# Optimization experiments

Hardware: AMD Instinct MI355X
Metric: run time of the kernel (lower is better)

Reference implementation:

```python
import jax, jax.numpy as jnp
import numpy as np

N_NODES = 100000
N_EDGES = 1000000
IN_CH, HID_CH, N_CLS = 128, 64, 40


def setup_inputs() -> dict:
    key = jax.random.key(0)
    ks = jax.random.split(key, 8)
    x = jax.random.normal(ks[0], (N_NODES, IN_CH), dtype=jnp.float32)
    edge_index = jax.random.randint(ks[1], (2, N_EDGES), 0, N_NODES, dtype=jnp.int32)
    # Glorot-ish scaled weights (ARMAConv init_weight / root_weight, K=1 stack squeezed)
    w1_init = jax.random.normal(ks[2], (IN_CH, HID_CH), dtype=jnp.float32) / np.sqrt(IN_CH)
    w1_root = jax.random.normal(ks[3], (IN_CH, HID_CH), dtype=jnp.float32) / np.sqrt(IN_CH)
    b1 = jnp.zeros((HID_CH,), dtype=jnp.float32)
    w2_init = jax.random.normal(ks[4], (HID_CH, N_CLS), dtype=jnp.float32) / np.sqrt(HID_CH)
    w2_root = jax.random.normal(ks[5], (HID_CH, N_CLS), dtype=jnp.float32) / np.sqrt(HID_CH)
    b2 = jnp.zeros((N_CLS,), dtype=jnp.float32)
    return {"x": x, "edge_index": edge_index,
            "w1_init": w1_init, "w1_root": w1_root, "b1": b1,
            "w2_init": w2_init, "w2_root": w2_root, "b2": b2}


def _arma_layer(x, row, col, norm, w_init, w_root, bias):
    # ARMAConv, num_stacks=1, num_layers=1, shared_weights=True, eval mode (dropout=id):
    # out = relu( A_hat @ (x W_init) + x W_root + b ), mean over the single stack.
    h = x @ w_init                           # [N, F_out]
    msg = norm[:, None] * h[row]             # gather from source nodes, [E, F_out]
    agg = jax.ops.segment_sum(msg, col, num_segments=N_NODES)  # scatter-add at targets
    return jax.nn.relu(agg + x @ w_root + bias)


def reference(x, edge_index, w1_init, w1_root, b1, w2_init, w2_root, b2):
    row, col = edge_index[0], edge_index[1]
    # gcn_norm, add_self_loops=False: deg over targets, norm = d^-1/2[row] * d^-1/2[col]
    deg = jax.ops.segment_sum(jnp.ones((row.shape[0],), x.dtype), col, num_segments=N_NODES)
    dinv = jnp.where(deg > 0, jax.lax.rsqrt(jnp.maximum(deg, 1e-12)), jnp.zeros_like(deg))
    norm = dinv[row] * dinv[col]
    h = _arma_layer(x, row, col, norm, w1_init, w1_root, b1)
    h = jax.nn.relu(h)  # BiARMA relu; dropout identity in eval
    return _arma_layer(h, row, col, norm, w2_init, w2_root, b2)
```

## Files before the change

### kernel.cpp

```cpp
#include <hip/hip_runtime.h>

#define N_NODES 100000
#define N_EDGES 1000000
#define IN_CH 128
#define HID_CH 64
#define N_CLS 40

#define NBUCK 782

static inline int cdiv(int a, int b) { return (a + b - 1) / b; }

using bf16x8 = __attribute__((ext_vector_type(8))) short;
using f32x4  = __attribute__((ext_vector_type(4))) float;

__device__ __forceinline__ unsigned pack_bf2(float a, float b) {
    unsigned ua = __float_as_uint(a), ub = __float_as_uint(b);
    ua += 0x7fffu + ((ua >> 16) & 1u);
    ub += 0x7fffu + ((ub >> 16) & 1u);
    return (ua >> 16) | (ub & 0xffff0000u);
}
__device__ __forceinline__ unsigned short bf16_of(float a) {
    unsigned ua = __float_as_uint(a);
    ua += 0x7fffu + ((ua >> 16) & 1u);
    return (unsigned short)(ua >> 16);
}
__device__ __forceinline__ float bf_lo(unsigned u) { return __uint_as_float(u << 16); }
__device__ __forceinline__ float bf_hi(unsigned u) { return __uint_as_float(u & 0xffff0000u); }


__global__ __launch_bounds__(256)
void bucket_count_wconv_kernel(const int* __restrict__ cols, int* __restrict__ gcount, int E,
                               const float* __restrict__ w1i, const float* __restrict__ w1r,
                               const float* __restrict__ w2i, const float* __restrict__ w2r,
                               unsigned* __restrict__ wtgA, unsigned* __restrict__ wtgB) {
    if (blockIdx.x >= 128) {
        if (wtgA == nullptr) return;
        int id = (blockIdx.x - 128) * 256 + threadIdx.x;
        if (id < 128 * 64) {
            int c = id >> 6, kp = id & 63;
            int k = kp * 2;
            const float* W = (c < 64) ? w1i : w1r;
            int cc = (c < 64) ? c : c - 64;
            float a = W[(size_t)k * 64 + cc];
            float b = W[(size_t)(k + 1) * 64 + cc];
            wtgA[c * 64 + kp] = pack_bf2(a, b);
        } else if (id < 128 * 64 + 80 * 32) {
            int j = id - 128 * 64;
            int c = j >> 5, kp = j & 31;
            int k = kp * 2;
            const float* W = (c < 40) ? w2i : w2r;
            int cc = (c < 40) ? c : c - 40;
            float a = W[(size_t)k * 40 + cc];
            float b = W[(size_t)(k + 1) * 40 + cc];
            wtgB[c * 32 + kp] = pack_bf2(a, b);
        }
        return;
    }
    __shared__ int hist[NBUCK];
    for (int i = threadIdx.x; i < NBUCK; i += 256) hist[i] = 0;
    __syncthreads();
    int per = (E + 127) / 128;
    int s = blockIdx.x * per;
    int e = min(E, s + per);
    for (int j = s + threadIdx.x; j < e; j += 256)
        atomicAdd(&hist[cols[j] >> 7], 1);
    __syncthreads();
    for (int i = threadIdx.x; i < NBUCK; i += 256)
        if (hist[i]) atomicAdd(&gcount[i], hist[i]);
}


__global__ __launch_bounds__(1024)
void scan_bucket_kernel(const int* __restrict__ gcount, int* __restrict__ boff,
                        int* __restrict__ gcursor, int* __restrict__ offsets) {
    __shared__ int part[1024];
    int t = threadIdx.x;
    part[t] = (t < NBUCK) ? gcount[t] : 0;
    __syncthreads();
    for (int off = 1; off < 1024; off <<= 1) {
        int v = (t >= off) ? part[t - off] : 0;
        __syncthreads();
        part[t] += v;
        __syncthreads();
    }
    int excl = (t > 0) ? part[t - 1] : 0;
    if (t < NBUCK) { boff[t] = excl; gcursor[t] = excl; }
    if (t == NBUCK) { boff[NBUCK] = excl; offsets[N_NODES] = excl; }
}


__global__ __launch_bounds__(256)
void bucket_scatter_kernel(const int* __restrict__ rows, const int* __restrict__ cols,
                           int* __restrict__ gcursor, int* __restrict__ pedge, int E) {
    __shared__ int cur[NBUCK];
    for (int i = threadIdx.x; i < NBUCK; i += 256) cur[i] = 0;
    __syncthreads();
    int per = (E + gridDim.x - 1) / gridDim.x;
    int s = blockIdx.x * per;
    int e = min(E, s + per);
    for (int j = s + threadIdx.x; j < e; j += 256)
        atomicAdd(&cur[cols[j] >> 7], 1);
    __syncthreads();
    for (int i = threadIdx.x; i < NBUCK; i += 256) {
        int h = cur[i];
        cur[i] = h ? atomicAdd(&gcursor[i], h) : 0;
    }
    __syncthreads();
    for (int j = s + threadIdx.x; j < e; j += 256) {
        int c = cols[j];
        int pos = atomicAdd(&cur[c >> 7], 1);
        pedge[pos] = (rows[j] << 7) | (c & 127);
    }
}


__global__ __launch_bounds__(256)
void bucket_sort_kernel(const int* __restrict__ boff, const int* __restrict__ pedge,
                        int* __restrict__ srow, int* __restrict__ offsets,
                        float* __restrict__ dinv) {
    __shared__ int cnt[128];
    __shared__ int scn[128];
    __shared__ int cur[128];
    int b = blockIdx.x, t = threadIdx.x;
    if (t < 128) cnt[t] = 0;
    __syncthreads();
    int e0 = boff[b], e1 = boff[b + 1];
    for (int j = e0 + t; j < e1; j += 256)
        atomicAdd(&cnt[pedge[j] & 127], 1);
    __syncthreads();
    if (t < 128) scn[t] = cnt[t];
    __syncthreads();
    for (int off = 1; off < 128; off <<= 1) {
        int v = 0;
        if (t < 128 && t >= off) v = scn[t - off];
        __syncthreads();
        if (t < 128) scn[t] += v;
        __syncthreads();
    }
    if (t < 128) {
        int excl = (t > 0) ? scn[t - 1] : 0;
        cur[t] = excl;
        int node = b * 128 + t;
        if (node < N_NODES) {
            offsets[node] = e0 + excl;
            dinv[node] = cnt[t] ? rsqrtf((float)cnt[t]) : 0.f;
        }
    }
    __syncthreads();
    for (int j = e0 + t; j < e1; j += 256) {
        int p = pedge[j];
        int pos = atomicAdd(&cur[p & 127], 1);
        srow[e0 + pos] = p >> 7;
    }
}


template<int K, int C1, int C2>
__launch_bounds__(256, 6)
__global__ void gemm_fat_kernel(const float* __restrict__ X,
                                const unsigned short* __restrict__ WT,
                                const float* __restrict__ Bias,
                                const float* __restrict__ dinv,
                                unsigned short* __restrict__ Y1b,
                                float* __restrict__ Y2, int N) {
    constexpr int CT = C1 + C2;
    constexpr int NT = CT / 16;
    constexpr int KS = K / 32;
    constexpr int S16 = 72;
    constexpr int SF  = 68;
    static_assert(CT % 16 == 0 && K % 32 == 0 && C1 % 8 == 0 && C2 % 4 == 0, "shape");

    __shared__ unsigned short eb16[4 * 16 * S16];
    __shared__ float          ebf [4 * 16 * SF];

    const int tid = threadIdx.x;
    const int wave = tid >> 6;
    const int lane = tid & 63;
    const int m = lane & 15;
    const int quad = lane >> 4;
    const int r0 = blockIdx.x * 64;

    const int rowA = r0 + wave * 16 + m;
    const bool va = (rowA < N);
    const float* xr = X + (size_t)rowA * K + quad * 8;

    union AFrag { uint4 u; bf16x8 v; } af[KS];
#pragma unroll
    for (int ks = 0; ks < KS; ++ks) {
        float4 v0 = make_float4(0.f, 0.f, 0.f, 0.f);
        float4 v1 = make_float4(0.f, 0.f, 0.f, 0.f);
        if (va) {
            v0 = *reinterpret_cast<const float4*>(xr + ks * 32);
            v1 = *reinterpret_cast<const float4*>(xr + ks * 32 + 4);
        }
        af[ks].u.x = pack_bf2(v0.x, v0.y);
        af[ks].u.y = pack_bf2(v0.z, v0.w);
        af[ks].u.z = pack_bf2(v1.x, v1.y);
        af[ks].u.w = pack_bf2(v1.z, v1.w);
    }

    f32x4 acc[NT];
#pragma unroll
    for (int t = 0; t < NT; ++t) acc[t] = (f32x4){0.f, 0.f, 0.f, 0.f};
#pragma unroll
    for (int ks = 0; ks < KS; ++ks) {
#pragma unroll
        for (int t = 0; t < NT; ++t) {
            bf16x8 b = *reinterpret_cast<const bf16x8*>(&WT[(size_t)(t * 16 + m) * K + ks * 32 + quad * 8]);
            acc[t] = __builtin_amdgcn_mfma_f32_16x16x32_bf16(af[ks].v, b, acc[t], 0, 0, 0);
        }
    }

    const int rbase0 = r0 + wave * 16;
    const int rbase = rbase0 + quad * 4;
    float dv[4];
#pragma unroll
    for (int reg = 0; reg < 4; ++reg)
        dv[reg] = (rbase + reg < N) ? dinv[rbase + reg] : 0.f;

    unsigned short* e16 = &eb16[wave * 16 * S16];
    float* ef = &ebf[wave * 16 * SF];
#pragma unroll
    for (int t = 0; t < NT; ++t) {
        int c = t * 16 + m;
        if (c < C1) {
#pragma unroll
            for (int reg = 0; reg < 4; ++reg)
                e16[(quad * 4 + reg) * S16 + c] = bf16_of(acc[t][reg] * dv[reg]);
        } else {
            float b = Bias[c - C1];
#pragma unroll
            for (int reg = 0; reg < 4; ++reg)
                ef[(quad * 4 + reg) * SF + (c - C1)] = acc[t][reg] + b;
        }
    }
    __syncthreads();

    constexpr int SEG1 = C1 / 8;
    for (int it = 0; it < (16 * SEG1 + 63) / 64; ++it) {
        int task = lane + it * 64;
        if (task < 16 * SEG1) {
            int row = task / SEG1, seg = task - row * SEG1;
            int gr = rbase0 + row;
            if (gr < N) {
                uint4 v = *reinterpret_cast<const uint4*>(&eb16[(wave * 16 + row) * S16 + seg * 8]);
                *reinterpret_cast<uint4*>(&Y1b[(size_t)gr * C1 + seg * 8]) = v;
            }
        }
    }
    constexpr int SEG2 = C2 / 4;
    for (int it = 0; it < (16 * SEG2 + 63) / 64; ++it) {
        int task = lane + it * 64;
        if (task < 16 * SEG2) {
            int row = task / SEG2, seg = task - row * SEG2;
            int gr = rbase0 + row;
            if (gr < N) {
                float4 v = *reinterpret_cast<const float4*>(&ebf[(wave * 16 + row) * SF + seg * 4]);
                *reinterpret_cast<float4*>(&Y2[(size_t)gr * C2 + seg * 4]) = v;
            }
        }
    }
}


__global__ __launch_bounds__(256)
void pull_gemm_fused_kernel(const int* __restrict__ offsets,
                            const int* __restrict__ srow,
                            const float* __restrict__ dinv,
                            const unsigned* __restrict__ H,
                            const float* __restrict__ Yp,
                            const unsigned short* __restrict__ WT2,
                            const float* __restrict__ Bias2,
                            unsigned short* __restrict__ H2,
                            float* __restrict__ Outp,
                            int N) {
    constexpr int KP = 36;
    __shared__ unsigned xb[16 * KP];
    __shared__ unsigned short e16[16 * 48];
    __shared__ float epif[16 * 44];

    const int tid = threadIdx.x;
    const int node16 = tid >> 4;
    const int lane16 = tid & 15;
    const int gnode = blockIdx.x * 16 + node16;

    float4 h1 = make_float4(0.f, 0.f, 0.f, 0.f);
    if (gnode < N) {
        int e0 = offsets[gnode];
        int e1 = offsets[gnode + 1];
        float dc = dinv[gnode];
        float4 acc = make_float4(0.f, 0.f, 0.f, 0.f);
        int j = e0;
        for (; j + 4 <= e1; j += 4) {
            int r0 = srow[j + 0];
            int r1 = srow[j + 1];
            int r2 = srow[j + 2];
            int r3 = srow[j + 3];
            uint2 u0 = *reinterpret_cast<const uint2*>(&H[(size_t)r0 * 32 + lane16 * 2]);
            uint2 u1 = *reinterpret_cast<const uint2*>(&H[(size_t)r1 * 32 + lane16 * 2]);
            uint2 u2 = *reinterpret_cast<const uint2*>(&H[(size_t)r2 * 32 + lane16 * 2]);
            uint2 u3 = *reinterpret_cast<const uint2*>(&H[(size_t)r3 * 32 + lane16 * 2]);
            acc.x += (bf_lo(u0.x) + bf_lo(u1.x)) + (bf_lo(u2.x) + bf_lo(u3.x));
            acc.y += (bf_hi(u0.x) + bf_hi(u1.x)) + (bf_hi(u2.x) + bf_hi(u3.x));
            acc.z += (bf_lo(u0.y) + bf_lo(u1.y)) + (bf_lo(u2.y) + bf_lo(u3.y));
            acc.w += (bf_hi(u0.y) + bf_hi(u1.y)) + (bf_hi(u2.y) + bf_hi(u3.y));
        }
        for (; j < e1; ++j) {
            int r = srow[j];
            uint2 u = *reinterpret_cast<const uint2*>(&H[(size_t)r * 32 + lane16 * 2]);
            acc.x += bf_lo(u.x);
            acc.y += bf_hi(u.x);
            acc.z += bf_lo(u.y);
            acc.w += bf_hi(u.y);
        }
        float4 y = *reinterpret_cast<const float4*>(&Yp[(size_t)gnode * 64 + lane16 * 4]);
        h1.x = fmaxf(fmaf(dc, acc.x, y.x), 0.f);
        h1.y = fmaxf(fmaf(dc, acc.y, y.y), 0.f);
        h1.z = fmaxf(fmaf(dc, acc.z, y.z), 0.f);
        h1.w = fmaxf(fmaf(dc, acc.w, y.w), 0.f);
    }
    xb[node16 * KP + lane16 * 2]     = pack_bf2(h1.x, h1.y);
    xb[node16 * KP + lane16 * 2 + 1] = pack_bf2(h1.z, h1.w);
    __syncthreads();

    const int wave = tid >> 6;
    const int lane = tid & 63;
    const int m = lane & 15;
    const int quad = lane >> 4;
    const int rb = blockIdx.x * 16 + quad * 4;

    float dv[4];
#pragma unroll
    for (int reg = 0; reg < 4; ++reg)
        dv[reg] = (rb + reg < N) ? dinv[rb + reg] : 0.f;

    bf16x8 a0 = *reinterpret_cast<const bf16x8*>(&xb[m * KP + 0 * 16 + quad * 4]);
    bf16x8 a1 = *reinterpret_cast<const bf16x8*>(&xb[m * KP + 1 * 16 + quad * 4]);

#pragma unroll
    for (int tt = 0; tt < 2; ++tt) {
        int t = wave + tt * 4;
        if (t >= 5) break;
        bf16x8 b0 = *reinterpret_cast<const bf16x8*>(&WT2[(t * 16 + m) * 64 + 0 * 32 + quad * 8]);
        bf16x8 b1 = *reinterpret_cast<const bf16x8*>(&WT2[(t * 16 + m) * 64 + 1 * 32 + quad * 8]);
        f32x4 acc2 = (f32x4){0.f, 0.f, 0.f, 0.f};
        acc2 = __builtin_amdgcn_mfma_f32_16x16x32_bf16(a0, b0, acc2, 0, 0, 0);
        acc2 = __builtin_amdgcn_mfma_f32_16x16x32_bf16(a1, b1, acc2, 0, 0, 0);
        int c = t * 16 + m;
        if (c < 40) {
#pragma unroll
            for (int reg = 0; reg < 4; ++reg)
                e16[(quad * 4 + reg) * 48 + c] = bf16_of(acc2[reg] * dv[reg]);
        } else {
            float bb = Bias2[c - 40];
#pragma unroll
            for (int reg = 0; reg < 4; ++reg)
                epif[(quad * 4 + reg) * 44 + (c - 40)] = acc2[reg] + bb;
        }
    }
    __syncthreads();

    if (tid < 80) {
        int row = tid / 5, seg = tid - row * 5;
        int gr = blockIdx.x * 16 + row;
        if (gr < N) {
            uint4 v = *reinterpret_cast<const uint4*>(&e16[row * 48 + seg * 8]);
            *reinterpret_cast<uint4*>(&H2[(size_t)gr * 40 + seg * 8]) = v;
        }
    }
    if (tid < 160) {
        int row = tid / 10, seg = tid - row * 10;
        int gr = blockIdx.x * 16 + row;
        if (gr < N) {
            float4 v = *reinterpret_cast<const float4*>(&epif[row * 44 + seg * 4]);
            *reinterpret_cast<float4*>(&Outp[(size_t)gr * 40 + seg * 4]) = v;
        }
    }
}


template<int K, int C1, int C2>
__launch_bounds__(256)
__global__ void gemm_mfma_fused_kernel(const float* __restrict__ X,
                                       const float* __restrict__ W1,
                                       const float* __restrict__ W2,
                                       const float* __restrict__ Bias,
                                       const float* __restrict__ dinv,
                                       unsigned short* __restrict__ Y1b,
                                       float* __restrict__ Y2, int N) {
    constexpr int CT = C1 + C2;
    constexpr int NT = CT / 16;
    constexpr int KS = K / 32;
    constexpr int KP = (K + 8) / 2;
    static_assert(CT % 16 == 0 && K % 32 == 0, "shape");
    static_assert(C1 % 4 == 0 && C2 % 4 == 0, "staging vec4");

    __shared__ unsigned xb[64 * KP];
    __shared__ unsigned wt[CT * KP];
    __shared__ float dloc[64];

    const int tid = threadIdx.x;
    const int wave = tid >> 6;
    const int lane = tid & 63;
    const int m = lane & 15;
    const int quad = lane >> 4;
    const int r0 = blockIdx.x * 64;

    if (tid < 64) {
        int gr = r0 + tid;
        dloc[tid] = (gr < N) ? dinv[gr] : 0.f;
    }

    constexpr int XIT = 64 * (K / 4);
    for (int i = tid; i < XIT; i += 256) {
        int rr = i / (K / 4);
        int k4 = i - rr * (K / 4);
        int gr = r0 + rr;
        float4 v = make_float4(0.f, 0.f, 0.f, 0.f);
        if (gr < N)
            v = *reinterpret_cast<const float4*>(&X[(size_t)gr * K + k4 * 4]);
        uint2 p;
        p.x = pack_bf2(v.x, v.y);
        p.y = pack_bf2(v.z, v.w);
        *reinterpret_cast<uint2*>(&xb[rr * KP + k4 * 2]) = p;
    }

    constexpr int WIT = (K / 2) * (CT / 4);
    for (int i = tid; i < WIT; i += 256) {
        int kp = i / (CT / 4);
        int c4 = i - kp * (CT / 4);
        int k = kp * 2;
        int c = c4 * 4;
        float4 va, vb;
        if (c < C1) {
            va = *reinterpret_cast<const float4*>(&W1[(size_t)k * C1 + c]);
            vb = *reinterpret_cast<const float4*>(&W1[(size_t)(k + 1) * C1 + c]);
        } else {
            va = *reinterpret_cast<const float4*>(&W2[(size_t)k * C2 + (c - C1)]);
            vb = *reinterpret_cast<const float4*>(&W2[(size_t)(k + 1) * C2 + (c - C1)]);
        }
        wt[(c + 0) * KP + kp] = pack_bf2(va.x, vb.x);
        wt[(c + 1) * KP + kp] = pack_bf2(va.y, vb.y);
        wt[(c + 2) * KP + kp] = pack_bf2(va.z, vb.z);
        wt[(c + 3) * KP + kp] = pack_bf2(va.w, vb.w);
    }
    __syncthreads();

    const int rowbase = wave * 16;
    f32x4 acc[NT];
#pragma unroll
    for (int t = 0; t < NT; ++t) acc[t] = (f32x4){0.f, 0.f, 0.f, 0.f};

#pragma unroll
    for (int ks = 0; ks < KS; ++ks) {
        bf16x8 a = *reinterpret_cast<const bf16x8*>(&xb[(rowbase + m) * KP + ks * 16 + quad * 4]);
#pragma unroll
        for (int t = 0; t < NT; ++t) {
            bf16x8 b = *reinterpret_cast<const bf16x8*>(&wt[(t * 16 + m) * KP + ks * 16 + quad * 4]);
            acc[t] = __builtin_amdgcn_mfma_f32_16x16x32_bf16(a, b, acc[t], 0, 0, 0);
        }
    }

#pragma unroll
    for (int t = 0; t < NT; ++t) {
        int c = t * 16 + m;
        float bias = (c >= C1) ? Bias[c - C1] : 0.f;
#pragma unroll
        for (int reg = 0; reg < 4; ++reg) {
            int rl = rowbase + quad * 4 + reg;
            int r = r0 + rl;
            if (r >= N) continue;
            float v = acc[t][reg];
            if (c < C1) {
                Y1b[(size_t)r * C1 + c] = bf16_of(v * dloc[rl]);
            } else {
                Y2[(size_t)r * C2 + (c - C1)] = v + bias;
            }
        }
    }
}


template<int C>
__launch_bounds__(256)
__global__ void pull_bf16_kernel(const int* __restrict__ offsets,
                                 const int* __restrict__ srow,
                                 const float* __restrict__ dinv,
                                 const unsigned* __restrict__ H,
                                 float* __restrict__ Y, int N) {
    constexpr int TPE = C / 4;
    constexpr int CH = C / 2;
    int gid = blockIdx.x * blockDim.x + threadIdx.x;
    int node = gid / TPE;
    int lane = gid - node * TPE;
    if (node >= N) return;

    int e0 = offsets[node];
    int e1 = offsets[node + 1];
    float dc = dinv[node];

    float4 acc = make_float4(0.f, 0.f, 0.f, 0.f);
    int j = e0;
    for (; j + 4 <= e1; j += 4) {
        int r0 = srow[j + 0];
        int r1 = srow[j + 1];
        int r2 = srow[j + 2];
        int r3 = srow[j + 3];
        uint2 u0 = *reinterpret_cast<const uint2*>(&H[(size_t)r0 * CH + lane * 2]);
        uint2 u1 = *reinterpret_cast<const uint2*>(&H[(size_t)r1 * CH + lane * 2]);
        uint2 u2 = *reinterpret_cast<const uint2*>(&H[(size_t)r2 * CH + lane * 2]);
        uint2 u3 = *reinterpret_cast<const uint2*>(&H[(size_t)r3 * CH + lane * 2]);
        acc.x += (bf_lo(u0.x) + bf_lo(u1.x)) + (bf_lo(u2.x) + bf_lo(u3.x));
        acc.y += (bf_hi(u0.x) + bf_hi(u1.x)) + (bf_hi(u2.x) + bf_hi(u3.x));
        acc.z += (bf_lo(u0.y) + bf_lo(u1.y)) + (bf_lo(u2.y) + bf_lo(u3.y));
        acc.w += (bf_hi(u0.y) + bf_hi(u1.y)) + (bf_hi(u2.y) + bf_hi(u3.y));
    }
    for (; j < e1; ++j) {
        int r = srow[j];
        uint2 u = *reinterpret_cast<const uint2*>(&H[(size_t)r * CH + lane * 2]);
        acc.x += bf_lo(u.x);
        acc.y += bf_hi(u.x);
        acc.z += bf_lo(u.y);
        acc.w += bf_hi(u.y);
    }

    float4* Y4 = reinterpret_cast<float4*>(Y);
    size_t yi = (size_t)node * TPE + lane;
    float4 y = Y4[yi];
    y.x = fmaxf(fmaf(dc, acc.x, y.x), 0.f);
    y.y = fmaxf(fmaf(dc, acc.y, y.y), 0.f);
    y.z = fmaxf(fmaf(dc, acc.z, y.z), 0.f);
    y.w = fmaxf(fmaf(dc, acc.w, y.w), 0.f);
    Y4[yi] = y;
}


extern "C" void kernel_launch(void* const* d_in, const int* in_sizes, int n_in,
                              void* d_out, int out_size, void* d_ws, size_t ws_size,
                              hipStream_t stream) {
    const float* x       = (const float*)d_in[0];
    const int*   eidx    = (const int*)d_in[1];
    const float* w1_init = (const float*)d_in[2];
    const float* w1_root = (const float*)d_in[3];
    const float* b1      = (const float*)d_in[4];
    const float* w2_init = (const float*)d_in[5];
    const float* w2_root = (const float*)d_in[6];
    const float* b2      = (const float*)d_in[7];
    float* out = (float*)d_out;

    const int* rows = eidx;
    const int* cols = eidx + N_EDGES;

    int* wsi = (int*)d_ws;
    int*      gcount  = wsi;
    int*      boff    = wsi + 784;
    int*      gcursor = wsi + 1572;
    float*    dinv    = (float*)(wsi + 2360);
    int*      offsets = wsi + 102360;
    int*      srow    = wsi + 202364;
    unsigned* h0b     = (unsigned*)(wsi + 1202364);
    int*      pedge   = wsi + 1202364;
    float*    agg1    = (float*)(wsi + 4402364);
    unsigned* h2b     = h0b;
    unsigned* wtgA    = (unsigned*)(wsi + 10802364);
    unsigned* wtgB    = wtgA + 8192;
    unsigned short* h2s = (unsigned short*)(wsi + 10813116);
    const size_t WS_B = 10813116ull * 4ull;
    const size_t WS_A = 12813116ull * 4ull;

    const bool have_wt = (ws_size >= WS_B);

    hipMemsetAsync(gcount, 0, 784 * sizeof(int), stream);
    bucket_count_wconv_kernel<<<170, 256, 0, stream>>>(
        cols, gcount, N_EDGES, w1_init, w1_root, w2_init, w2_root,
        have_wt ? wtgA : nullptr, have_wt ? wtgB : nullptr);
    scan_bucket_kernel<<<1, 1024, 0, stream>>>(gcount, boff, gcursor, offsets);
    bucket_scatter_kernel<<<128, 256, 0, stream>>>(rows, cols, gcursor, pedge, N_EDGES);
    bucket_sort_kernel<<<NBUCK, 256, 0, stream>>>(boff, pedge, srow, offsets, dinv);

    const int NTILES = cdiv(N_NODES, 64);

    if (ws_size >= WS_A) {
        gemm_fat_kernel<IN_CH, HID_CH, HID_CH><<<NTILES, 256, 0, stream>>>(
            x, (const unsigned short*)wtgA, b1, dinv, (unsigned short*)h0b, agg1, N_NODES);
        pull_gemm_fused_kernel<<<cdiv(N_NODES, 16), 256, 0, stream>>>(
            offsets, srow, dinv, h0b, agg1, (const unsigned short*)wtgB, b2,
            h2s, out, N_NODES);
        pull_bf16_kernel<N_CLS><<<cdiv(N_NODES * (N_CLS / 4), 256), 256, 0, stream>>>(
            offsets, srow, dinv, (const unsigned*)h2s, out, N_NODES);
    } else if (have_wt) {
        gemm_fat_kernel<IN_CH, HID_CH, HID_CH><<<NTILES, 256, 0, stream>>>(
            x, (const unsigned short*)wtgA, b1, dinv, (unsigned short*)h0b, agg1, N_NODES);
        pull_bf16_kernel<HID_CH><<<cdiv(N_NODES * (HID_CH / 4), 256), 256, 0, stream>>>(
            offsets, srow, dinv, h0b, agg1, N_NODES);
        gemm_fat_kernel<HID_CH, N_CLS, N_CLS><<<NTILES, 256, 0, stream>>>(
            agg1, (const unsigned short*)wtgB, b2, dinv, (unsigned short*)h2b, out, N_NODES);
        pull_bf16_kernel<N_CLS><<<cdiv(N_NODES * (N_CLS / 4), 256), 256, 0, stream>>>(
            offsets, srow, dinv, h2b, out, N_NODES);
    } else {
        gemm_mfma_fused_kernel<IN_CH, HID_CH, HID_CH><<<NTILES, 256, 0, stream>>>(
            x, w1_init, w1_root, b1, dinv, (unsigned short*)h0b, agg1, N_NODES);
        pull_bf16_kernel<HID_CH><<<cdiv(N_NODES * (HID_CH / 4), 256), 256, 0, stream>>>(
            offsets, srow, dinv, h0b, agg1, N_NODES);
        gemm_mfma_fused_kernel<HID_CH, N_CLS, N_CLS><<<NTILES, 256, 0, stream>>>(
            agg1, w2_init, w2_root, b2, dinv, (unsigned short*)h2b, out, N_NODES);
        pull_bf16_kernel<N_CLS><<<cdiv(N_NODES * (N_CLS / 4), 256), 256, 0, stream>>>(
            offsets, srow, dinv, h2b, out, N_NODES);
    }
}
```

Baseline: 252.9 us.

## Fuse CSR preprocessing stages into one cooperative kernel with grid syncs

Replaces the memset plus four preprocessing launches (bucket count, scan, scatter, per-bucket sort) with one cooperative kernel of 782 blocks that separates the phases with grid.sync(). The scan now runs in 256 threads with four elements each. The aim is to remove launch gaps and the idle tail between small kernels. In exchange it relies on all 782 blocks being co-resident, adds grid-wide barrier costs, and falls back to the old multi-kernel path if the cooperative launch fails.

```diff
diff --git a/kernel.cpp b/kernel.cpp
--- a/kernel.cpp
+++ b/kernel.cpp
@@ -1,4 +1,7 @@
 #include <hip/hip_runtime.h>
+#include <hip/hip_cooperative_groups.h>
+
+namespace cg = cooperative_groups;
 
 #define N_NODES 100000
 #define N_EDGES 1000000
@@ -26,6 +29,156 @@
 }
 __device__ __forceinline__ float bf_lo(unsigned u) { return __uint_as_float(u << 16); }
 __device__ __forceinline__ float bf_hi(unsigned u) { return __uint_as_float(u & 0xffff0000u); }
+
+
+__device__ __forceinline__ void wconv_item(int id,
+                                           const float* __restrict__ w1i, const float* __restrict__ w1r,
+                                           const float* __restrict__ w2i, const float* __restrict__ w2r,
+                                           unsigned* __restrict__ wtgA, unsigned* __restrict__ wtgB) {
+    if (id < 128 * 64) {
+        int c = id >> 6, kp = id & 63;
+        int k = kp * 2;
+        const float* W = (c < 64) ? w1i : w1r;
+        int cc = (c < 64) ? c : c - 64;
+        float a = W[(size_t)k * 64 + cc];
+        float b = W[(size_t)(k + 1) * 64 + cc];
+        wtgA[c * 64 + kp] = pack_bf2(a, b);
+    } else if (id < 128 * 64 + 80 * 32) {
+        int j = id - 128 * 64;
+        int c = j >> 5, kp = j & 31;
+        int k = kp * 2;
+        const float* W = (c < 40) ? w2i : w2r;
+        int cc = (c < 40) ? c : c - 40;
+        float a = W[(size_t)k * 40 + cc];
+        float b = W[(size_t)(k + 1) * 40 + cc];
+        wtgB[c * 32 + kp] = pack_bf2(a, b);
+    }
+}
+
+
+__global__ __launch_bounds__(256)
+void prep_all_kernel(const int* __restrict__ rows, const int* __restrict__ cols,
+                     int* __restrict__ gcount, int* __restrict__ boff,
+                     int* __restrict__ gcursor, int* __restrict__ pedge,
+                     int* __restrict__ srow, int* __restrict__ offsets,
+                     float* __restrict__ dinv,
+                     const float* __restrict__ w1i, const float* __restrict__ w1r,
+                     const float* __restrict__ w2i, const float* __restrict__ w2r,
+                     unsigned* __restrict__ wtgA, unsigned* __restrict__ wtgB) {
+    cg::grid_group grid = cg::this_grid();
+    __shared__ int hist[NBUCK];
+    __shared__ int sc[256];
+    __shared__ int cnt[128];
+    __shared__ int scn[128];
+    __shared__ int cur[128];
+
+    const int bid = blockIdx.x;
+    const int t = threadIdx.x;
+    constexpr int E = N_EDGES;
+
+    if (bid == 0) {
+        for (int i = t; i < NBUCK; i += 256) gcount[i] = 0;
+    } else if (bid >= 1 && bid <= 42 && wtgA != nullptr) {
+        wconv_item((bid - 1) * 256 + t, w1i, w1r, w2i, w2r, wtgA, wtgB);
+    }
+    grid.sync();
+
+    if (bid < 128) {
+        for (int i = t; i < NBUCK; i += 256) hist[i] = 0;
+        __syncthreads();
+        int per = (E + 127) / 128;
+        int s = bid * per;
+        int e = min(E, s + per);
+        for (int j = s + t; j < e; j += 256)
+            atomicAdd(&hist[cols[j] >> 7], 1);
+        __syncthreads();
+        for (int i = t; i < NBUCK; i += 256)
+            if (hist[i]) atomicAdd(&gcount[i], hist[i]);
+    }
+    grid.sync();
+
+    if (bid == 0) {
+        int base = t * 4;
+        int v0 = (base + 0 < NBUCK) ? gcount[base + 0] : 0;
+        int v1 = (base + 1 < NBUCK) ? gcount[base + 1] : 0;
+        int v2 = (base + 2 < NBUCK) ? gcount[base + 2] : 0;
+        int v3 = (base + 3 < NBUCK) ? gcount[base + 3] : 0;
+        sc[t] = v0 + v1 + v2 + v3;
+        __syncthreads();
+        for (int off = 1; off < 256; off <<= 1) {
+            int val = (t >= off) ? sc[t - off] : 0;
+            __syncthreads();
+            sc[t] += val;
+            __syncthreads();
+        }
+        int e0 = (t > 0) ? sc[t - 1] : 0;
+        int e1 = e0 + v0;
+        int e2 = e1 + v1;
+        int e3 = e2 + v2;
+        if (base + 0 < NBUCK) { boff[base + 0] = e0; gcursor[base + 0] = e0; }
+        if (base + 1 < NBUCK) { boff[base + 1] = e1; gcursor[base + 1] = e1; }
+        if (base + 2 < NBUCK) { boff[base + 2] = e2; gcursor[base + 2] = e2; }
+        if (base + 3 < NBUCK) { boff[base + 3] = e3; gcursor[base + 3] = e3; }
+        if (t == 255) { boff[NBUCK] = sc[255]; offsets[N_NODES] = sc[255]; }
+    }
+    grid.sync();
+
+    if (bid < 128) {
+        for (int i = t; i < NBUCK; i += 256) hist[i] = 0;
+        __syncthreads();
+        int per = (E + 127) / 128;
+        int s = bid * per;
+        int e = min(E, s + per);
+        for (int j = s + t; j < e; j += 256)
+            atomicAdd(&hist[cols[j] >> 7], 1);
+        __syncthreads();
+        for (int i = t; i < NBUCK; i += 256) {
+            int h = hist[i];
+            hist[i] = h ? atomicAdd(&gcursor[i], h) : 0;
+        }
+        __syncthreads();
+        for (int j = s + t; j < e; j += 256) {
+            int c = cols[j];
+            int pos = atomicAdd(&hist[c >> 7], 1);
+            pedge[pos] = (rows[j] << 7) | (c & 127);
+        }
+    }
+    grid.sync();
+
+    {
+        int b = bid;
+        if (t < 128) cnt[t] = 0;
+        __syncthreads();
+        int e0 = boff[b], e1 = boff[b + 1];
+        for (int j = e0 + t; j < e1; j += 256)
+            atomicAdd(&cnt[pedge[j] & 127], 1);
+        __syncthreads();
+        if (t < 128) scn[t] = cnt[t];
+        __syncthreads();
+        for (int off = 1; off < 128; off <<= 1) {
+            int v = 0;
+            if (t < 128 && t >= off) v = scn[t - off];
+            __syncthreads();
+            if (t < 128) scn[t] += v;
+            __syncthreads();
+        }
+        if (t < 128) {
+            int excl = (t > 0) ? scn[t - 1] : 0;
+            cur[t] = excl;
+            int node = b * 128 + t;
+            if (node < N_NODES) {
+                offsets[node] = e0 + excl;
+                dinv[node] = cnt[t] ? rsqrtf((float)cnt[t]) : 0.f;
+            }
+        }
+        __syncthreads();
+        for (int j = e0 + t; j < e1; j += 256) {
+            int p = pedge[j];
+            int pos = atomicAdd(&cur[p & 127], 1);
+            srow[e0 + pos] = p >> 7;
+        }
+    }
+}
 
 
 __global__ __launch_bounds__(256)
@@ -35,25 +188,7 @@
                                unsigned* __restrict__ wtgA, unsigned* __restrict__ wtgB) {
     if (blockIdx.x >= 128) {
         if (wtgA == nullptr) return;
-        int id = (blockIdx.x - 128) * 256 + threadIdx.x;
-        if (id < 128 * 64) {
-            int c = id >> 6, kp = id & 63;
-            int k = kp * 2;
-            const float* W = (c < 64) ? w1i : w1r;
-            int cc = (c < 64) ? c : c - 64;
-            float a = W[(size_t)k * 64 + cc];
-            float b = W[(size_t)(k + 1) * 64 + cc];
-            wtgA[c * 64 + kp] = pack_bf2(a, b);
-        } else if (id < 128 * 64 + 80 * 32) {
-            int j = id - 128 * 64;
-            int c = j >> 5, kp = j & 31;
-            int k = kp * 2;
-            const float* W = (c < 40) ? w2i : w2r;
-            int cc = (c < 40) ? c : c - 40;
-            float a = W[(size_t)k * 40 + cc];
-            float b = W[(size_t)(k + 1) * 40 + cc];
-            wtgB[c * 32 + kp] = pack_bf2(a, b);
-        }
+        wconv_item((blockIdx.x - 128) * 256 + threadIdx.x, w1i, w1r, w2i, w2r, wtgA, wtgB);
         return;
     }
     __shared__ int hist[NBUCK];
@@ -68,7 +203,6 @@
     for (int i = threadIdx.x; i < NBUCK; i += 256)
         if (hist[i]) atomicAdd(&gcount[i], hist[i]);
 }
-
 
 __global__ __launch_bounds__(1024)
 void scan_bucket_kernel(const int* __restrict__ gcount, int* __restrict__ boff,
@@ -88,7 +222,6 @@
     if (t == NBUCK) { boff[NBUCK] = excl; offsets[N_NODES] = excl; }
 }
 
-
 __global__ __launch_bounds__(256)
 void bucket_scatter_kernel(const int* __restrict__ rows, const int* __restrict__ cols,
                            int* __restrict__ gcursor, int* __restrict__ pedge, int E) {
@@ -112,7 +245,6 @@
         pedge[pos] = (rows[j] << 7) | (c & 127);
     }
 }
-
 
 __global__ __launch_bounds__(256)
 void bucket_sort_kernel(const int* __restrict__ boff, const int* __restrict__ pedge,
@@ -569,14 +701,31 @@
     const size_t WS_A = 12813116ull * 4ull;
 
     const bool have_wt = (ws_size >= WS_B);
-
-    hipMemsetAsync(gcount, 0, 784 * sizeof(int), stream);
-    bucket_count_wconv_kernel<<<170, 256, 0, stream>>>(
-        cols, gcount, N_EDGES, w1_init, w1_root, w2_init, w2_root,
-        have_wt ? wtgA : nullptr, have_wt ? wtgB : nullptr);
-    scan_bucket_kernel<<<1, 1024, 0, stream>>>(gcount, boff, gcursor, offsets);
-    bucket_scatter_kernel<<<128, 256, 0, stream>>>(rows, cols, gcursor, pedge, N_EDGES);
-    bucket_sort_kernel<<<NBUCK, 256, 0, stream>>>(boff, pedge, srow, offsets, dinv);
+    unsigned* wtgA_arg = have_wt ? wtgA : nullptr;
+    unsigned* wtgB_arg = have_wt ? wtgB : nullptr;
+
+    bool coop_ok = false;
+    {
+        void* args[] = {
+            (void*)&rows, (void*)&cols, (void*)&gcount, (void*)&boff,
+            (void*)&gcursor, (void*)&pedge, (void*)&srow, (void*)&offsets,
+            (void*)&dinv, (void*)&w1_init, (void*)&w1_root, (void*)&w2_init,
+            (void*)&w2_root, (void*)&wtgA_arg, (void*)&wtgB_arg
+        };
+        hipError_t cerr = hipLaunchCooperativeKernel(
+            reinterpret_cast<void*>(prep_all_kernel),
+            dim3(NBUCK), dim3(256), args, 0, stream);
+        coop_ok = (cerr == hipSuccess);
+    }
+    if (!coop_ok) {
+        hipMemsetAsync(gcount, 0, 784 * sizeof(int), stream);
+        bucket_count_wconv_kernel<<<170, 256, 0, stream>>>(
+            cols, gcount, N_EDGES, w1_init, w1_root, w2_init, w2_root,
+            wtgA_arg, wtgB_arg);
+        scan_bucket_kernel<<<1, 1024, 0, stream>>>(gcount, boff, gcursor, offsets);
+        bucket_scatter_kernel<<<128, 256, 0, stream>>>(rows, cols, gcursor, pedge, N_EDGES);
+        bucket_sort_kernel<<<NBUCK, 256, 0, stream>>>(boff, pedge, srow, offsets, dinv);
+    }
 
     const int NTILES = cdiv(N_NODES, 64);
 
```

After: 553.6 us. +118.9%, slower.
